# Kernel optimization log

Hardware: AMD Instinct MI355X
Metric: run time of the kernel (lower is better)

The kernel has to match this reference:

```python
import jax, jax.numpy as jnp
import numpy as np

IN_FEATURES = 8192
OUT_FEATURES = 8192
POOL_K = 16
SCALE = 2.0


def setup_inputs() -> dict:
    key = jax.random.key(0)
    k1, k2, k3 = jax.random.split(key, 3)
    B = 4096
    x = jax.random.normal(k1, (B, IN_FEATURES), dtype=jnp.float32)
    # nn.Linear default init: U(-1/sqrt(fan_in), 1/sqrt(fan_in))
    bound = 1.0 / np.sqrt(IN_FEATURES)
    W = jax.random.uniform(k2, (OUT_FEATURES, IN_FEATURES), dtype=jnp.float32, minval=-bound, maxval=bound)
    b = jax.random.uniform(k3, (OUT_FEATURES,), dtype=jnp.float32, minval=-bound, maxval=bound)
    return {"x": x, "W": W, "b": b}


def reference(x, W, b):
    # GEMM: [B, C_out]
    y = jnp.dot(x, W.T) + b
    B, C = y.shape
    # AvgPool1d over feature dim, kernel=stride=POOL_K -> [B, C/POOL_K]
    pooled = y.reshape(B, C // POOL_K, POOL_K).mean(axis=-1)
    # GELU (tanh approximation) + scale, then row-wise max -> [B]
    v = jax.nn.gelu(pooled, approximate=True) * SCALE
    return jnp.max(v, axis=-1)
```

## Files before the change

### kernel.cpp

```cpp
#include <hip/hip_runtime.h>
#include <hip/hip_bf16.h>
#include <cmath>

#define M_DIM 4096
#define N_POOL 512
#define K_DIM 8192
#define KSPLIT 8
#define K_PER (K_DIM / KSPLIT)

typedef __bf16 bf16x8 __attribute__((ext_vector_type(8)));
typedef float floatx4 __attribute__((ext_vector_type(4)));
typedef unsigned short ushort8v __attribute__((ext_vector_type(8)));

__device__ __forceinline__ unsigned short f2bf(float f) {
  unsigned int u = __float_as_uint(f);
  return (unsigned short)((u + 0x7fffu + ((u >> 16) & 1u)) >> 16);
}

__global__ void convert_f32_bf16(const float4* __restrict__ src,
                                 ushort8v* __restrict__ dst, int n8) {
  int i = blockIdx.x * blockDim.x + threadIdx.x;
  int stride = gridDim.x * blockDim.x;
  for (; i < n8; i += stride) {
    float4 a = src[2 * i], b = src[2 * i + 1];
    ushort8v o;
    o[0] = f2bf(a.x); o[1] = f2bf(a.y); o[2] = f2bf(a.z); o[3] = f2bf(a.w);
    o[4] = f2bf(b.x); o[5] = f2bf(b.y); o[6] = f2bf(b.z); o[7] = f2bf(b.w);
    dst[i] = o;
  }
}

__global__ void wpool_kernel(const float* __restrict__ W,
                             unsigned short* __restrict__ Wp) {
  int g = blockIdx.x;
  const float* base = W + (size_t)g * 16 * K_DIM;
  ushort4* out = (ushort4*)(Wp + (size_t)g * K_DIM);
  for (int c4 = threadIdx.x; c4 < K_DIM / 4; c4 += blockDim.x) {
    float4 s = {0.f, 0.f, 0.f, 0.f};
#pragma unroll
    for (int j = 0; j < 16; ++j) {
      float4 v = ((const float4*)(base + (size_t)j * K_DIM))[c4];
      s.x += v.x; s.y += v.y; s.z += v.z; s.w += v.w;
    }
    ushort4 o;
    o.x = f2bf(s.x); o.y = f2bf(s.y); o.z = f2bf(s.z); o.w = f2bf(s.w);
    out[c4] = o;
  }
}

__global__ void bias_pool(const float* __restrict__ b, float* __restrict__ bpool) {
  int g = threadIdx.x;
  float s = 0.f;
  for (int i = 0; i < 16; ++i) s += b[g * 16 + i];
  bpool[g] = s;
}

__global__ __launch_bounds__(256) void gemm_splitk(
    const unsigned short* __restrict__ xb,
    const unsigned short* __restrict__ wp,
    float* __restrict__ part)
{
  __shared__ __align__(16) unsigned short As[128 * 64];
  __shared__ __align__(16) unsigned short Bs[128 * 64];

  const int tid = threadIdx.x;
  const int L = tid & 63;
  const int w = tid >> 6;
  const int wm = w & 1, wn = w >> 1;
  const int lane15 = L & 15, quad = L >> 4;

  const int bn = blockIdx.x, bm = blockIdx.y, kz = blockIdx.z;

  const int srow = w * 32 + (L >> 3);
  const int schunk = ((L & 7) ^ ((L >> 3) & 7)) * 8;
  const unsigned short* ga = xb + (size_t)(bm * 128 + srow) * K_DIM + kz * K_PER + schunk;
  const unsigned short* gb = wp + (size_t)(bn * 128 + srow) * K_DIM + kz * K_PER + schunk;
  unsigned short* lA = As + (w * 32) * 64;
  unsigned short* lB = Bs + (w * 32) * 64;

  floatx4 acc[4][4];
#pragma unroll
  for (int t = 0; t < 4; ++t)
#pragma unroll
    for (int u = 0; u < 4; ++u) acc[t][u] = (floatx4)0.f;

  const bf16x8* Av = (const bf16x8*)As;
  const bf16x8* Bv = (const bf16x8*)Bs;

  for (int kk = 0; kk < K_PER / 64; ++kk) {
#pragma unroll
    for (int i = 0; i < 4; ++i) {
      __builtin_amdgcn_global_load_lds(
          (const __attribute__((address_space(1))) void*)(ga + (size_t)(i * 8) * K_DIM),
          (__attribute__((address_space(3))) void*)(lA + i * 8 * 64), 16, 0, 0);
    }
#pragma unroll
    for (int i = 0; i < 4; ++i) {
      __builtin_amdgcn_global_load_lds(
          (const __attribute__((address_space(1))) void*)(gb + (size_t)(i * 8) * K_DIM),
          (__attribute__((address_space(3))) void*)(lB + i * 8 * 64), 16, 0, 0);
    }
    ga += 64; gb += 64;
    __syncthreads();

#pragma unroll
    for (int ks = 0; ks < 2; ++ks) {
      bf16x8 af[4], bfr[4];
#pragma unroll
      for (int t = 0; t < 4; ++t) {
        int r = wm * 64 + t * 16 + lane15;
        af[t] = Av[r * 8 + ((ks * 4 + quad) ^ (lane15 & 7))];
      }
#pragma unroll
      for (int u = 0; u < 4; ++u) {
        int r = wn * 64 + u * 16 + lane15;
        bfr[u] = Bv[r * 8 + ((ks * 4 + quad) ^ (lane15 & 7))];
      }
#pragma unroll
      for (int t = 0; t < 4; ++t)
#pragma unroll
        for (int u = 0; u < 4; ++u)
          acc[t][u] = __builtin_amdgcn_mfma_f32_16x16x32_bf16(af[t], bfr[u],
                                                              acc[t][u], 0, 0, 0);
    }
    __syncthreads();
  }

  float* cp = part + (size_t)kz * M_DIM * N_POOL;
  const int row_base = bm * 128 + wm * 64;
  const int col_base = bn * 128 + wn * 64;
#pragma unroll
  for (int t = 0; t < 4; ++t)
#pragma unroll
    for (int u = 0; u < 4; ++u) {
      int col = col_base + u * 16 + lane15;
#pragma unroll
      for (int r = 0; r < 4; ++r) {
        int row = row_base + t * 16 + quad * 4 + r;
        cp[(size_t)row * N_POOL + col] = acc[t][u][r];
      }
    }
}

__global__ void finalize(const float* __restrict__ part,
                         const float* __restrict__ bpool,
                         float* __restrict__ out) {
  int row = blockIdx.x;
  int lane = threadIdx.x;
  float mx = -INFINITY;
#pragma unroll
  for (int j = 0; j < 8; ++j) {
    int g = lane + j * 64;
    float s = bpool[g];
#pragma unroll
    for (int kz = 0; kz < KSPLIT; ++kz)
      s += part[(size_t)kz * M_DIM * N_POOL + (size_t)row * N_POOL + g];
    float p = s * 0.0625f;
    float t = tanhf(0.7978845608028654f * (p + 0.044715f * p * p * p));
    mx = fmaxf(mx, p * (1.0f + t));
  }
#pragma unroll
  for (int s = 32; s >= 1; s >>= 1) mx = fmaxf(mx, __shfl_xor(mx, s));
  if (lane == 0) out[row] = mx;
}

extern "C" void kernel_launch(void* const* d_in, const int* in_sizes, int n_in,
                              void* d_out, int out_size, void* d_ws, size_t ws_size,
                              hipStream_t stream) {
  const float* x = (const float*)d_in[0];
  const float* W = (const float*)d_in[1];
  const float* b = (const float*)d_in[2];
  float* out = (float*)d_out;

  char* ws = (char*)d_ws;
  unsigned short* xb = (unsigned short*)ws;
  unsigned short* Wp = (unsigned short*)(ws + (size_t)67108864);
  float* part = (float*)(ws + (size_t)75497472);
  float* bpool = (float*)(ws + (size_t)142606336);

  wpool_kernel<<<N_POOL, 256, 0, stream>>>(W, Wp);
  convert_f32_bf16<<<2048, 256, 0, stream>>>((const float4*)x, (ushort8v*)xb,
                                             (M_DIM * K_DIM) / 8);
  bias_pool<<<1, 512, 0, stream>>>(b, bpool);

  dim3 grid(N_POOL / 128, M_DIM / 128, KSPLIT);
  gemm_splitk<<<grid, 256, 0, stream>>>(xb, Wp, part);

  finalize<<<M_DIM, 64, 0, stream>>>(part, bpool, out);
}
```

Measured before the change: 515.1 us.

## Replace split-K partial buffers with atomic accumulation into bias-initialized pooled output

The GEMM epilogue now atomically adds each split-K slice into one pooled buffer that is pre-initialized with the pooled bias. This removes the 8-way partial buffer writes and the finalize kernel's reduction reads. The W pooling kernel also gets a 2D grid for more parallelism. In exchange it adds float atomics, which introduce contention and make the summation order nondeterministic, plus an extra init kernel.

```diff
diff --git a/kernel.cpp b/kernel.cpp
--- a/kernel.cpp
+++ b/kernel.cpp
@@ -35,7 +35,9 @@
   int g = blockIdx.x;
   const float* base = W + (size_t)g * 16 * K_DIM;
   ushort4* out = (ushort4*)(Wp + (size_t)g * K_DIM);
-  for (int c4 = threadIdx.x; c4 < K_DIM / 4; c4 += blockDim.x) {
+  int c4 = blockIdx.y * 512 + threadIdx.x;
+#pragma unroll
+  for (int it = 0; it < 2; ++it, c4 += 256) {
     float4 s = {0.f, 0.f, 0.f, 0.f};
 #pragma unroll
     for (int j = 0; j < 16; ++j) {
@@ -55,10 +57,16 @@
   bpool[g] = s;
 }
 
+__global__ void init_pooled(const float4* __restrict__ bpool4,
+                            float4* __restrict__ pooled4) {
+  int i = blockIdx.x * blockDim.x + threadIdx.x;
+  pooled4[i] = bpool4[i & 127];
+}
+
 __global__ __launch_bounds__(256) void gemm_splitk(
     const unsigned short* __restrict__ xb,
     const unsigned short* __restrict__ wp,
-    float* __restrict__ part)
+    float* __restrict__ pooled)
 {
   __shared__ __align__(16) unsigned short As[128 * 64];
   __shared__ __align__(16) unsigned short Bs[128 * 64];
@@ -126,7 +134,6 @@
     __syncthreads();
   }
 
-  float* cp = part + (size_t)kz * M_DIM * N_POOL;
   const int row_base = bm * 128 + wm * 64;
   const int col_base = bn * 128 + wn * 64;
 #pragma unroll
@@ -137,25 +144,20 @@
 #pragma unroll
       for (int r = 0; r < 4; ++r) {
         int row = row_base + t * 16 + quad * 4 + r;
-        cp[(size_t)row * N_POOL + col] = acc[t][u][r];
+        atomicAdd(&pooled[(size_t)row * N_POOL + col], acc[t][u][r]);
       }
     }
 }
 
-__global__ void finalize(const float* __restrict__ part,
-                         const float* __restrict__ bpool,
+__global__ void finalize(const float* __restrict__ pooled,
                          float* __restrict__ out) {
   int row = blockIdx.x;
   int lane = threadIdx.x;
+  const float* pr = pooled + (size_t)row * N_POOL;
   float mx = -INFINITY;
 #pragma unroll
   for (int j = 0; j < 8; ++j) {
-    int g = lane + j * 64;
-    float s = bpool[g];
-#pragma unroll
-    for (int kz = 0; kz < KSPLIT; ++kz)
-      s += part[(size_t)kz * M_DIM * N_POOL + (size_t)row * N_POOL + g];
-    float p = s * 0.0625f;
+    float p = pr[lane + j * 64] * 0.0625f;
     float t = tanhf(0.7978845608028654f * (p + 0.044715f * p * p * p));
     mx = fmaxf(mx, p * (1.0f + t));
   }
@@ -175,16 +177,18 @@
   char* ws = (char*)d_ws;
   unsigned short* xb = (unsigned short*)ws;
   unsigned short* Wp = (unsigned short*)(ws + (size_t)67108864);
-  float* part = (float*)(ws + (size_t)75497472);
-  float* bpool = (float*)(ws + (size_t)142606336);
+  float* pooled = (float*)(ws + (size_t)75497472);
+  float* bpool = (float*)(ws + (size_t)83886080);
 
-  wpool_kernel<<<N_POOL, 256, 0, stream>>>(W, Wp);
+  bias_pool<<<1, 512, 0, stream>>>(b, bpool);
+  init_pooled<<<(M_DIM * N_POOL / 4) / 256, 256, 0, stream>>>(
+      (const float4*)bpool, (float4*)pooled);
+  wpool_kernel<<<dim3(N_POOL, 4), 256, 0, stream>>>(W, Wp);
   convert_f32_bf16<<<2048, 256, 0, stream>>>((const float4*)x, (ushort8v*)xb,
                                              (M_DIM * K_DIM) / 8);
-  bias_pool<<<1, 512, 0, stream>>>(b, bpool);
 
   dim3 grid(N_POOL / 128, M_DIM / 128, KSPLIT);
-  gemm_splitk<<<grid, 256, 0, stream>>>(xb, Wp, part);
+  gemm_splitk<<<grid, 256, 0, stream>>>(xb, Wp, pooled);
 
-  finalize<<<M_DIM, 64, 0, stream>>>(part, bpool, out);
+  finalize<<<M_DIM, 64, 0, stream>>>(pooled, out);
 }
```

Result: slower. 538.2 us (+4.5%).
